# Optimization experiments

Measured on AMD Instinct MI355X. Metric: run time of the kernel, lower is better.

Reference implementation:

```python
import jax, jax.numpy as jnp
import numpy as np

N_HEAD = 16


def setup_inputs() -> dict:
    key = jax.random.key(0)
    k1, k2, k3 = jax.random.split(key, 3)
    B, T, C = 2, 2048, 1024
    x = jax.random.normal(k1, (B, T, C), dtype=jnp.float32)
    attention_mask = jnp.zeros((B, 1, 1, T), dtype=jnp.float32)
    W_attn = jax.random.normal(k2, (C, 3 * C), dtype=jnp.float32) * 0.02
    b_attn = jnp.zeros((3 * C,), dtype=jnp.float32)
    W_proj = jax.random.normal(k3, (C, C), dtype=jnp.float32) * 0.02
    b_proj = jnp.zeros((C,), dtype=jnp.float32)
    return {"x": x, "attention_mask": attention_mask, "W_attn": W_attn,
            "b_attn": b_attn, "W_proj": W_proj, "b_proj": b_proj}


def reference(x, attention_mask, W_attn, b_attn, W_proj, b_proj):
    B, T, C = x.shape
    H = N_HEAD
    d = C // H
    qkv = x @ W_attn + b_attn                      # [B, T, 3C]
    q, k, v = jnp.split(qkv, 3, axis=-1)
    q = q.reshape(B, T, H, d).transpose(0, 2, 1, 3)  # [B, H, T, d]
    k = k.reshape(B, T, H, d).transpose(0, 2, 1, 3)
    v = v.reshape(B, T, H, d).transpose(0, 2, 1, 3)
    att = jnp.einsum('bhtd,bhsd->bhts', q, k) * (1.0 / np.sqrt(d))
    causal = jnp.tril(jnp.ones((T, T), dtype=bool))
    att = jnp.where(causal[None, None], att, jnp.float32(-10000.0))
    att = att + attention_mask                     # additive broadcast mask
    att = jax.nn.softmax(att, axis=-1)             # dropout p=0.0 -> identity
    y = jnp.einsum('bhts,bhsd->bhtd', att, v)      # [B, H, T, d]
    y = y.transpose(0, 2, 1, 3).reshape(B, T, C)
    return y @ W_proj + b_proj
```

## Files before the change

### kernel.cpp

```cpp
#include <hip/hip_runtime.h>
#include <hip/hip_bf16.h>
#include <stdint.h>

#define BATCH 2
#define TT 2048
#define CC 1024
#define NH 16
#define HD 64

typedef __attribute__((ext_vector_type(8))) short short8;
typedef __attribute__((ext_vector_type(4))) short sh4;
typedef __attribute__((ext_vector_type(4))) float f32x4;
typedef __attribute__((ext_vector_type(2))) unsigned uint2v;

#define MFMA16 __builtin_amdgcn_mfma_f32_16x16x32_bf16
#define LOG2E 1.4426950408889634f

#if defined(__has_builtin)
#if __has_builtin(__builtin_amdgcn_exp2f)
#define EXP2(x) __builtin_amdgcn_exp2f(x)
#else
#define EXP2(x) __expf((x) * 0.6931471805599453f)
#endif
#else
#define EXP2(x) __expf((x) * 0.6931471805599453f)
#endif

__device__ __forceinline__ short f2bf(float f) {
  union { float f; unsigned u; } x;
  x.f = f;
  unsigned r = x.u + 0x7FFFu + ((x.u >> 16) & 1u);
  return (short)(r >> 16);
}

__device__ __forceinline__ void transpose_cast_tile(
    const float* __restrict__ W, short* __restrict__ Wt, int K, int N,
    int n0, int k0, int tid) {
  __shared__ __align__(16) float Ls[64][68];
  {
    const int r = tid >> 4, c4 = (tid & 15) * 4;
#pragma unroll
    for (int p = 0; p < 4; ++p) {
      const float4 v = *reinterpret_cast<const float4*>(
          &W[(size_t)(k0 + r + p * 16) * N + n0 + c4]);
      *reinterpret_cast<float4*>(&Ls[r + p * 16][c4]) = v;
    }
  }
  __syncthreads();
  {
    const int n = tid >> 2;
    const int kk0 = (tid & 3) * 16;
#pragma unroll
    for (int half = 0; half < 2; ++half) {
      short8 o;
#pragma unroll
      for (int t = 0; t < 8; ++t) o[t] = f2bf(Ls[kk0 + half * 8 + t][n]);
      *reinterpret_cast<short8*>(&Wt[(size_t)(n0 + n) * K + k0 + kk0 + half * 8]) = o;
    }
  }
}

__global__ __launch_bounds__(256) void prep_fused(
    const float* __restrict__ x, short* __restrict__ xb,
    const float* __restrict__ W_attn, short* __restrict__ wat,
    const float* __restrict__ W_proj, short* __restrict__ wpt,
    const float* __restrict__ mask, short* __restrict__ cb16,
    float* __restrict__ cf32) {
  const int blk = blockIdx.x;
  const int tid = threadIdx.x;
  if (blk < 2048) {
    const int i = (blk * 256 + tid) * 8;
    const float4 a = *reinterpret_cast<const float4*>(&x[i]);
    const float4 b = *reinterpret_cast<const float4*>(&x[i + 4]);
    short8 o;
    o[0] = f2bf(a.x); o[1] = f2bf(a.y); o[2] = f2bf(a.z); o[3] = f2bf(a.w);
    o[4] = f2bf(b.x); o[5] = f2bf(b.y); o[6] = f2bf(b.z); o[7] = f2bf(b.w);
    *reinterpret_cast<short8*>(&xb[i]) = o;
  } else if (blk < 2816) {
    const int b2 = blk - 2048;
    transpose_cast_tile(W_attn, wat, CC, 3 * CC, (b2 % 48) * 64,
                        (b2 / 48) * 64, tid);
  } else if (blk < 3072) {
    const int b3 = blk - 2816;
    transpose_cast_tile(W_proj, wpt, CC, CC, (b3 % 16) * 64, (b3 / 16) * 64,
                        tid);
  } else {
    const int b = blk - 3072;
    const int s = tid * 8;
    float c[8];
#pragma unroll
    for (int t = 0; t < 8; ++t) c[t] = __expf(mask[b * TT + s + t]);
    short8 o;
#pragma unroll
    for (int t = 0; t < 8; ++t) o[t] = f2bf(c[t]);
    *reinterpret_cast<short8*>(&cb16[b * TT + s]) = o;
#pragma unroll
    for (int t = 0; t < 8; ++t) cf32[b * TT + s + t] = c[t];
  }
}

template <bool OUT_BF16>
__device__ __forceinline__ void gemm_bt_body(
    const short* __restrict__ A, const short* __restrict__ Bt,
    const float* __restrict__ bias, void* __restrict__ C,
    short* __restrict__ vT, const float* __restrict__ cV, int M, int N, int K,
    int QS) {
  __shared__ __align__(16) short SM[24576];
  short* As = SM;
  short* Bs = SM + 8192;
  const int tid = threadIdx.x;
  const int w = tid >> 6, lane = tid & 63;
  const int quad = lane >> 4, l15 = lane & 15;
  const int m0 = blockIdx.y * 64, n0 = blockIdx.x * 128;

  f32x4 acc[4][2] = {};
  const int row16 = lane >> 2;
  const int c4 = (lane & 3) * 8;

  const int rbaseA = __builtin_amdgcn_readfirstlane(w * 16);
  const int rbaseB0 = __builtin_amdgcn_readfirstlane(w * 2 * 16);
  const int rbaseB1 = __builtin_amdgcn_readfirstlane((w * 2 + 1) * 16);

#define STAGE_TILE(buf, k0)                                                    \
  {                                                                            \
    _Pragma("unroll") for (int kh = 0; kh < 2; ++kh) {                         \
      const short* ga =                                                        \
          &A[(size_t)(m0 + rbaseA + row16) * K + (k0) + kh * 32 + c4];         \
      __builtin_amdgcn_global_load_lds(                                        \
          (const __attribute__((address_space(1))) void*)ga,                   \
          (__attribute__((address_space(3))) void*)                            \
              &As[(buf)*4096 + kh * 2048 + rbaseA * 32],                       \
          16, 0, 0);                                                           \
      const short* gb0 =                                                       \
          &Bt[(size_t)(n0 + rbaseB0 + row16) * K + (k0) + kh * 32 + c4];       \
      __builtin_amdgcn_global_load_lds(                                        \
          (const __attribute__((address_space(1))) void*)gb0,                  \
          (__attribute__((address_space(3))) void*)                            \
              &Bs[(buf)*8192 + kh * 4096 + rbaseB0 * 32],                      \
          16, 0, 0);                                                           \
      const short* gb1 =                                                       \
          &Bt[(size_t)(n0 + rbaseB1 + row16) * K + (k0) + kh * 32 + c4];       \
      __builtin_amdgcn_global_load_lds(                                        \
          (const __attribute__((address_space(1))) void*)gb1,                  \
          (__attribute__((address_space(3))) void*)                            \
              &Bs[(buf)*8192 + kh * 4096 + rbaseB1 * 32],                      \
          16, 0, 0);                                                           \
    }                                                                          \
  }

  STAGE_TILE(0, 0)
  __syncthreads();

  int cur = 0;
  for (int k0 = 0; k0 < K; k0 += 64) {
    if (k0 + 64 < K) STAGE_TILE(cur ^ 1, k0 + 64)

    short8 af[2][4], bfr[2][2];
#pragma unroll
    for (int kh = 0; kh < 2; ++kh) {
#pragma unroll
      for (int i = 0; i < 4; ++i)
        af[kh][i] = *reinterpret_cast<const short8*>(
            &As[cur * 4096 + kh * 2048 + (i * 16 + l15) * 32 + quad * 8]);
#pragma unroll
      for (int j = 0; j < 2; ++j)
        bfr[kh][j] = *reinterpret_cast<const short8*>(
            &Bs[cur * 8192 + kh * 4096 + (w * 32 + j * 16 + l15) * 32 +
                quad * 8]);
    }
#pragma unroll
    for (int kh = 0; kh < 2; ++kh)
#pragma unroll
      for (int i = 0; i < 4; ++i)
#pragma unroll
        for (int j = 0; j < 2; ++j)
          acc[i][j] = MFMA16(af[kh][i], bfr[kh][j], acc[i][j], 0, 0, 0);

    __syncthreads();
    cur ^= 1;
  }
#undef STAGE_TILE

  if (OUT_BF16 && vT != nullptr && n0 >= 2 * CC) {
    const int n0v = n0 - 2 * CC;
    const int b = m0 >> 11;
    const int s_batch = m0 & (TT - 1);
    short* Ls = SM;
#pragma unroll
    for (int i = 0; i < 4; ++i) {
      const int sl = i * 16 + quad * 4;
      const float4 cv = *reinterpret_cast<const float4*>(&cV[m0 + sl]);
      const float cvr[4] = {cv.x, cv.y, cv.z, cv.w};
#pragma unroll
      for (int j = 0; j < 2; ++j) {
        const int dl = w * 32 + j * 16 + l15;
        const float bb = bias[n0 + dl];
        sh4 pw;
#pragma unroll
        for (int r = 0; r < 4; ++r)
          pw[r] = f2bf((acc[i][j][r] + bb) * cvr[r]);
        *reinterpret_cast<sh4*>(&Ls[dl * 88 + sl]) = pw;
      }
    }
    __syncthreads();
    {
      const int row = tid >> 1, seg = tid & 1;
      const int bh = b * 16 + (n0v >> 6) + (row >> 6);
      const int d = row & 63;
      const short8* src = reinterpret_cast<const short8*>(&Ls[row * 88 + seg * 32]);
      short8* dst = reinterpret_cast<short8*>(
          &vT[((size_t)(bh * HD + d)) * TT + s_batch + seg * 32]);
#pragma unroll
      for (int t = 0; t < 4; ++t) dst[t] = src[t];
    }
    return;
  }

#pragma unroll
  for (int i = 0; i < 4; ++i) {
#pragma unroll
    for (int r = 0; r < 4; ++r) {
      const int row = m0 + i * 16 + quad * 4 + r;
#pragma unroll
      for (int j = 0; j < 2; ++j) {
        const int col = n0 + w * 32 + j * 16 + l15;
        float v = acc[i][j][r] + bias[col];
        if (col < QS) v *= 0.18033688011112042f;
        if (OUT_BF16)
          ((short*)C)[(size_t)row * N + col] = f2bf(v);
        else
          ((float*)C)[(size_t)row * N + col] = v;
      }
    }
  }
}

__global__ __launch_bounds__(256) void gemm_qkv(
    const short* __restrict__ A, const short* __restrict__ Bt,
    const float* __restrict__ bias, void* __restrict__ C,
    short* __restrict__ vT, const float* __restrict__ cV, int M, int N, int K,
    int QS) {
  gemm_bt_body<true>(A, Bt, bias, C, vT, cV, M, N, K, QS);
}

__global__ __launch_bounds__(256) void gemm_proj(
    const short* __restrict__ A, const short* __restrict__ Bt,
    const float* __restrict__ bias, void* __restrict__ C, int M, int N,
    int K) {
  gemm_bt_body<false>(A, Bt, bias, C, nullptr, nullptr, M, N, K, 0);
}

#define PST 72
__global__ __launch_bounds__(256) void attn_mfma10(
    const short* __restrict__ qkv, const short* __restrict__ vT,
    const short* __restrict__ cb16, short* __restrict__ y) {
  __shared__ __align__(16) short Ks[2][64 * PST];
  __shared__ __align__(16) short Vs[2][64 * PST];
  __shared__ __align__(16) short Ps[64 * PST];
  __shared__ __align__(16) short Cs[2][64];
  const int tid = threadIdx.x;
  const int w = tid >> 6, lane = tid & 63;
  const int quad = lane >> 4, l15 = lane & 15;
  const int bh = blockIdx.x, b = bh >> 4, h = bh & 15;
  const int px = blockIdx.y;
  const int qh = 31 - px;
  const int nth = qh + 1;
  const int ntot = nth + px + 1;
  const int RS = 3 * CC;

  int qt = qh;
  int qrow0 = qt * 64 + w * 16;

  short8 qf0, qf1;
  {
    const size_t qrow = (size_t)(b * TT + qrow0 + l15) * RS + h * HD + quad * 8;
    qf0 = *reinterpret_cast<const short8*>(&qkv[qrow]);
    qf1 = *reinterpret_cast<const short8*>(&qkv[qrow + 32]);
  }

  f32x4 l_acc = {};
  f32x4 o_acc[4] = {};

  const int sr = tid >> 3, sc = (tid & 7) * 8;
  const short* kbase = qkv + (size_t)(b * TT + sr) * RS + CC + h * HD + sc;
  const short* vbase = vT + (size_t)(bh * HD + sr) * TT + sc;
  const short* cbase = cb16 + b * TT;
  short* psrow = &Ps[(w * 16 + l15) * PST];
  const int kfo0 = quad * 8, kfo1 = 32 + quad * 8;

  short8 kpre0 = *reinterpret_cast<const short8*>(kbase);
  short8 kpre1 = *reinterpret_cast<const short8*>(kbase + (size_t)32 * RS);
  short8 vpre0 = *reinterpret_cast<const short8*>(vbase);
  short8 vpre1 = *reinterpret_cast<const short8*>(vbase + 32 * TT);
  short8 cpre = {};
  if (tid < 8) cpre = *reinterpret_cast<const short8*>(&cbase[tid * 8]);

  for (int it = 0; it < ntot; ++it) {
    const int kt = (it < nth) ? it : it - nth;
    const int s0 = kt * 64;

    if (it == nth) {
#pragma unroll
      for (int r = 0; r < 4; ++r) {
        const float inv = 1.0f / l_acc[r];
        const size_t row = (size_t)(b * TT + qrow0 + quad * 4 + r);
#pragma unroll
        for (int t = 0; t < 4; ++t)
          y[row * CC + h * HD + t * 16 + l15] = f2bf(o_acc[t][r] * inv);
      }
      qt = px;
      qrow0 = qt * 64 + w * 16;
      const size_t qrow = (size_t)(b * TT + qrow0 + l15) * RS + h * HD + quad * 8;
      qf0 = *reinterpret_cast<const short8*>(&qkv[qrow]);
      qf1 = *reinterpret_cast<const short8*>(&qkv[qrow + 32]);
      l_acc = f32x4{0.f, 0.f, 0.f, 0.f};
#pragma unroll
      for (int t = 0; t < 4; ++t) o_acc[t] = f32x4{0.f, 0.f, 0.f, 0.f};
    }

    const int cur = it & 1;
    *reinterpret_cast<short8*>(&Ks[cur][sr * PST + sc]) = kpre0;
    *reinterpret_cast<short8*>(&Ks[cur][(sr + 32) * PST + sc]) = kpre1;
    *reinterpret_cast<short8*>(&Vs[cur][sr * PST + sc]) = vpre0;
    *reinterpret_cast<short8*>(&Vs[cur][(sr + 32) * PST + sc]) = vpre1;
    if (tid < 8) *reinterpret_cast<short8*>(&Cs[cur][tid * 8]) = cpre;
    __syncthreads();

    if (it + 1 < ntot) {
      const int ktn = (it + 1 == nth) ? 0 : kt + 1;
      const short* kp = kbase + (size_t)ktn * 64 * RS;
      const short* vp = vbase + ktn * 64;
      kpre0 = *reinterpret_cast<const short8*>(kp);
      kpre1 = *reinterpret_cast<const short8*>(kp + (size_t)32 * RS);
      vpre0 = *reinterpret_cast<const short8*>(vp);
      vpre1 = *reinterpret_cast<const short8*>(vp + 32 * TT);
      if (tid < 8)
        cpre = *reinterpret_cast<const short8*>(&cbase[ktn * 64 + tid * 8]);
    }

    f32x4 sa[4] = {};
#pragma unroll
    for (int j = 0; j < 4; ++j) {
      const short8 kf0 = *reinterpret_cast<const short8*>(
          &Ks[cur][(j * 16 + l15) * PST + kfo0]);
      const short8 kf1 = *reinterpret_cast<const short8*>(
          &Ks[cur][(j * 16 + l15) * PST + kfo1]);
      sa[j] = MFMA16(kf0, qf0, sa[j], 0, 0, 0);
      sa[j] = MFMA16(kf1, qf1, sa[j], 0, 0, 0);
    }

    const bool boundary = (kt == qt);
    const int qg = qrow0 + l15;
#pragma unroll
    for (int j = 0; j < 4; ++j) {
      float pv[4];
#pragma unroll
      for (int r = 0; r < 4; ++r) {
        float v = sa[j][r];
        if (boundary) {
          const int sg = s0 + j * 16 + quad * 4 + r;
          if (sg > qg) v = -10000.0f;
        }
        pv[r] = EXP2(v);
      }
      union { __hip_bfloat162 h2[2]; uint2v u; } pk;
      pk.h2[0] = __float22bfloat162_rn(make_float2(pv[0], pv[1]));
      pk.h2[1] = __float22bfloat162_rn(make_float2(pv[2], pv[3]));
      *reinterpret_cast<uint2v*>(&psrow[j * 16 + quad * 4]) = pk.u;
    }

    const short8 pf0 = *reinterpret_cast<const short8*>(&psrow[kfo0]);
    const short8 pf1 = *reinterpret_cast<const short8*>(&psrow[kfo1]);
    const short8 cf0 = *reinterpret_cast<const short8*>(&Cs[cur][kfo0]);
    const short8 cf1 = *reinterpret_cast<const short8*>(&Cs[cur][kfo1]);
    l_acc = MFMA16(pf0, cf0, l_acc, 0, 0, 0);
    l_acc = MFMA16(pf1, cf1, l_acc, 0, 0, 0);
#pragma unroll
    for (int t = 0; t < 4; ++t) {
      const short8 vf0 = *reinterpret_cast<const short8*>(
          &Vs[cur][(t * 16 + l15) * PST + kfo0]);
      const short8 vf1 = *reinterpret_cast<const short8*>(
          &Vs[cur][(t * 16 + l15) * PST + kfo1]);
      o_acc[t] = MFMA16(pf0, vf0, o_acc[t], 0, 0, 0);
      o_acc[t] = MFMA16(pf1, vf1, o_acc[t], 0, 0, 0);
    }
  }

#pragma unroll
  for (int r = 0; r < 4; ++r) {
    const float inv = 1.0f / l_acc[r];
    const size_t row = (size_t)(b * TT + qrow0 + quad * 4 + r);
#pragma unroll
    for (int t = 0; t < 4; ++t)
      y[row * CC + h * HD + t * 16 + l15] = f2bf(o_acc[t][r] * inv);
  }
}

extern "C" void kernel_launch(void* const* d_in, const int* in_sizes, int n_in,
                              void* d_out, int out_size, void* d_ws,
                              size_t ws_size, hipStream_t stream) {
  const float* x = (const float*)d_in[0];
  const float* attn_mask = (const float*)d_in[1];
  const float* W_attn = (const float*)d_in[2];
  const float* b_attn = (const float*)d_in[3];
  const float* W_proj = (const float*)d_in[4];
  const float* b_proj = (const float*)d_in[5];
  float* out = (float*)d_out;

  const int M = BATCH * TT;

  short* xb = (short*)d_ws;
  short* wat = xb + (size_t)M * CC;
  short* wpt = wat + (size_t)(3 * CC) * CC;
  short* qkvb = wpt + (size_t)CC * CC;
  short* yb = qkvb + (size_t)M * 3 * CC;
  short* vTb = yb + (size_t)M * CC;
  short* cb16 = vTb + (size_t)BATCH * NH * HD * TT;
  float* cf32 = (float*)(cb16 + (size_t)BATCH * TT);

  prep_fused<<<3074, 256, 0, stream>>>(x, xb, W_attn, wat, W_proj, wpt,
                                       attn_mask, cb16, cf32);

  gemm_qkv<<<dim3((3 * CC) / 128, M / 64), 256, 0, stream>>>(
      xb, wat, b_attn, qkvb, vTb, cf32, M, 3 * CC, CC, CC);

  attn_mfma10<<<dim3(BATCH * NH, 16), 256, 0, stream>>>(
      qkvb, vTb, cb16, yb);

  gemm_proj<<<dim3(CC / 128, M / 64), 256, 0, stream>>>(
      yb, wpt, b_proj, out, M, CC, CC);
}
```

Measured before the change: 181.7 us.

## Software-pipeline attention: defer PV matmul one iteration behind QK and softmax

```diff
diff --git a/kernel.cpp b/kernel.cpp
--- a/kernel.cpp
+++ b/kernel.cpp
@@ -251,13 +251,13 @@
 }
 
 #define PST 72
-__global__ __launch_bounds__(256) void attn_mfma10(
+__global__ __launch_bounds__(256) void attn_mfma11(
     const short* __restrict__ qkv, const short* __restrict__ vT,
     const short* __restrict__ cb16, short* __restrict__ y) {
   __shared__ __align__(16) short Ks[2][64 * PST];
-  __shared__ __align__(16) short Vs[2][64 * PST];
-  __shared__ __align__(16) short Ps[64 * PST];
-  __shared__ __align__(16) short Cs[2][64];
+  __shared__ __align__(16) short Vs[3][64 * PST];
+  __shared__ __align__(16) short Ps[2][64 * PST];
+  __shared__ __align__(16) short Cs[3][64];
   const int tid = threadIdx.x;
   const int w = tid >> 6, lane = tid & 63;
   const int quad = lane >> 4, l15 = lane & 15;
@@ -285,8 +285,27 @@
   const short* kbase = qkv + (size_t)(b * TT + sr) * RS + CC + h * HD + sc;
   const short* vbase = vT + (size_t)(bh * HD + sr) * TT + sc;
   const short* cbase = cb16 + b * TT;
-  short* psrow = &Ps[(w * 16 + l15) * PST];
+  const int psoff = (w * 16 + l15) * PST;
   const int kfo0 = quad * 8, kfo1 = 32 + quad * 8;
+
+  auto pv_step = [&](int p2, int p3) {
+    const short* ppr = &Ps[p2][psoff];
+    const short8 pf0 = *reinterpret_cast<const short8*>(&ppr[kfo0]);
+    const short8 pf1 = *reinterpret_cast<const short8*>(&ppr[kfo1]);
+    const short8 cf0 = *reinterpret_cast<const short8*>(&Cs[p3][kfo0]);
+    const short8 cf1 = *reinterpret_cast<const short8*>(&Cs[p3][kfo1]);
+    l_acc = MFMA16(pf0, cf0, l_acc, 0, 0, 0);
+    l_acc = MFMA16(pf1, cf1, l_acc, 0, 0, 0);
+#pragma unroll
+    for (int t = 0; t < 4; ++t) {
+      const short8 vf0 = *reinterpret_cast<const short8*>(
+          &Vs[p3][(t * 16 + l15) * PST + kfo0]);
+      const short8 vf1 = *reinterpret_cast<const short8*>(
+          &Vs[p3][(t * 16 + l15) * PST + kfo1]);
+      o_acc[t] = MFMA16(pf0, vf0, o_acc[t], 0, 0, 0);
+      o_acc[t] = MFMA16(pf1, vf1, o_acc[t], 0, 0, 0);
+    }
+  };
 
   short8 kpre0 = *reinterpret_cast<const short8*>(kbase);
   short8 kpre1 = *reinterpret_cast<const short8*>(kbase + (size_t)32 * RS);
@@ -298,8 +317,17 @@
   for (int it = 0; it < ntot; ++it) {
     const int kt = (it < nth) ? it : it - nth;
     const int s0 = kt * 64;
+    const int cur2 = it & 1, cur3 = it % 3;
+    const int prv2 = cur2 ^ 1, prv3 = (it + 2) % 3;
+
+    *reinterpret_cast<short8*>(&Ks[cur2][sr * PST + sc]) = kpre0;
+    *reinterpret_cast<short8*>(&Ks[cur2][(sr + 32) * PST + sc]) = kpre1;
+    *reinterpret_cast<short8*>(&Vs[cur3][sr * PST + sc]) = vpre0;
+    *reinterpret_cast<short8*>(&Vs[cur3][(sr + 32) * PST + sc]) = vpre1;
+    if (tid < 8) *reinterpret_cast<short8*>(&Cs[cur3][tid * 8]) = cpre;
 
     if (it == nth) {
+      pv_step(prv2, prv3);
 #pragma unroll
       for (int r = 0; r < 4; ++r) {
         const float inv = 1.0f / l_acc[r];
@@ -317,13 +345,6 @@
 #pragma unroll
       for (int t = 0; t < 4; ++t) o_acc[t] = f32x4{0.f, 0.f, 0.f, 0.f};
     }
-
-    const int cur = it & 1;
-    *reinterpret_cast<short8*>(&Ks[cur][sr * PST + sc]) = kpre0;
-    *reinterpret_cast<short8*>(&Ks[cur][(sr + 32) * PST + sc]) = kpre1;
-    *reinterpret_cast<short8*>(&Vs[cur][sr * PST + sc]) = vpre0;
-    *reinterpret_cast<short8*>(&Vs[cur][(sr + 32) * PST + sc]) = vpre1;
-    if (tid < 8) *reinterpret_cast<short8*>(&Cs[cur][tid * 8]) = cpre;
     __syncthreads();
 
     if (it + 1 < ntot) {
@@ -342,15 +363,18 @@
 #pragma unroll
     for (int j = 0; j < 4; ++j) {
       const short8 kf0 = *reinterpret_cast<const short8*>(
-          &Ks[cur][(j * 16 + l15) * PST + kfo0]);
+          &Ks[cur2][(j * 16 + l15) * PST + kfo0]);
       const short8 kf1 = *reinterpret_cast<const short8*>(
-          &Ks[cur][(j * 16 + l15) * PST + kfo1]);
+          &Ks[cur2][(j * 16 + l15) * PST + kfo1]);
       sa[j] = MFMA16(kf0, qf0, sa[j], 0, 0, 0);
       sa[j] = MFMA16(kf1, qf1, sa[j], 0, 0, 0);
     }
 
+    if (it != nth && it > 0) pv_step(prv2, prv3);
+
     const bool boundary = (kt == qt);
     const int qg = qrow0 + l15;
+    short* psc = &Ps[cur2][psoff];
 #pragma unroll
     for (int j = 0; j < 4; ++j) {
       float pv[4];
@@ -366,26 +390,11 @@
       union { __hip_bfloat162 h2[2]; uint2v u; } pk;
       pk.h2[0] = __float22bfloat162_rn(make_float2(pv[0], pv[1]));
       pk.h2[1] = __float22bfloat162_rn(make_float2(pv[2], pv[3]));
-      *reinterpret_cast<uint2v*>(&psrow[j * 16 + quad * 4]) = pk.u;
-    }
-
-    const short8 pf0 = *reinterpret_cast<const short8*>(&psrow[kfo0]);
-    const short8 pf1 = *reinterpret_cast<const short8*>(&psrow[kfo1]);
-    const short8 cf0 = *reinterpret_cast<const short8*>(&Cs[cur][kfo0]);
-    const short8 cf1 = *reinterpret_cast<const short8*>(&Cs[cur][kfo1]);
-    l_acc = MFMA16(pf0, cf0, l_acc, 0, 0, 0);
-    l_acc = MFMA16(pf1, cf1, l_acc, 0, 0, 0);
-#pragma unroll
-    for (int t = 0; t < 4; ++t) {
-      const short8 vf0 = *reinterpret_cast<const short8*>(
-          &Vs[cur][(t * 16 + l15) * PST + kfo0]);
-      const short8 vf1 = *reinterpret_cast<const short8*>(
-          &Vs[cur][(t * 16 + l15) * PST + kfo1]);
-      o_acc[t] = MFMA16(pf0, vf0, o_acc[t], 0, 0, 0);
-      o_acc[t] = MFMA16(pf1, vf1, o_acc[t], 0, 0, 0);
-    }
-  }
-
+      *reinterpret_cast<uint2v*>(&psc[j * 16 + quad * 4]) = pk.u;
+    }
+  }
+
+  pv_step((ntot - 1) & 1, (ntot - 1) % 3);
 #pragma unroll
   for (int r = 0; r < 4; ++r) {
     const float inv = 1.0f / l_acc[r];
@@ -424,7 +433,7 @@
   gemm_qkv<<<dim3((3 * CC) / 128, M / 64), 256, 0, stream>>>(
       xb, wat, b_attn, qkvb, vTb, cf32, M, 3 * CC, CC, CC);
 
-  attn_mfma10<<<dim3(BATCH * NH, 16), 256, 0, stream>>>(
+  attn_mfma11<<<dim3(BATCH * NH, 16), 256, 0, stream>>>(
       qkvb, vTb, cb16, yb);
 
   gemm_proj<<<dim3(CC / 128, M / 64), 256, 0, stream>>>(
```

Measured after the change: 184.4 us. Within noise of the previous version (+1.5%).

## Load K/V fragments directly from global into registers, drop LDS staging

Applied to the files above, without the earlier changes.

```diff
diff --git a/kernel.cpp b/kernel.cpp
--- a/kernel.cpp
+++ b/kernel.cpp
@@ -251,13 +251,10 @@
 }
 
 #define PST 72
-__global__ __launch_bounds__(256) void attn_mfma10(
+__global__ __launch_bounds__(256) void attn_mfma12(
     const short* __restrict__ qkv, const short* __restrict__ vT,
     const short* __restrict__ cb16, short* __restrict__ y) {
-  __shared__ __align__(16) short Ks[2][64 * PST];
-  __shared__ __align__(16) short Vs[2][64 * PST];
   __shared__ __align__(16) short Ps[64 * PST];
-  __shared__ __align__(16) short Cs[2][64];
   const int tid = threadIdx.x;
   const int w = tid >> 6, lane = tid & 63;
   const int quad = lane >> 4, l15 = lane & 15;
@@ -281,19 +278,19 @@
   f32x4 l_acc = {};
   f32x4 o_acc[4] = {};
 
-  const int sr = tid >> 3, sc = (tid & 7) * 8;
-  const short* kbase = qkv + (size_t)(b * TT + sr) * RS + CC + h * HD + sc;
-  const short* vbase = vT + (size_t)(bh * HD + sr) * TT + sc;
-  const short* cbase = cb16 + b * TT;
+  const short* kgb = qkv + (size_t)b * TT * RS + CC + h * HD + quad * 8;
+  const short* vgb = vT + (size_t)bh * HD * TT + quad * 8;
+  const short* cgb = cb16 + b * TT + quad * 8;
   short* psrow = &Ps[(w * 16 + l15) * PST];
   const int kfo0 = quad * 8, kfo1 = 32 + quad * 8;
 
-  short8 kpre0 = *reinterpret_cast<const short8*>(kbase);
-  short8 kpre1 = *reinterpret_cast<const short8*>(kbase + (size_t)32 * RS);
-  short8 vpre0 = *reinterpret_cast<const short8*>(vbase);
-  short8 vpre1 = *reinterpret_cast<const short8*>(vbase + 32 * TT);
-  short8 cpre = {};
-  if (tid < 8) cpre = *reinterpret_cast<const short8*>(&cbase[tid * 8]);
+  short8 kf[4][2];
+#pragma unroll
+  for (int j = 0; j < 4; ++j) {
+    const short* kp = kgb + (size_t)(j * 16 + l15) * RS;
+    kf[j][0] = *reinterpret_cast<const short8*>(kp);
+    kf[j][1] = *reinterpret_cast<const short8*>(kp + 32);
+  }
 
   for (int it = 0; it < ntot; ++it) {
     const int kt = (it < nth) ? it : it - nth;
@@ -318,35 +315,31 @@
       for (int t = 0; t < 4; ++t) o_acc[t] = f32x4{0.f, 0.f, 0.f, 0.f};
     }
 
-    const int cur = it & 1;
-    *reinterpret_cast<short8*>(&Ks[cur][sr * PST + sc]) = kpre0;
-    *reinterpret_cast<short8*>(&Ks[cur][(sr + 32) * PST + sc]) = kpre1;
-    *reinterpret_cast<short8*>(&Vs[cur][sr * PST + sc]) = vpre0;
-    *reinterpret_cast<short8*>(&Vs[cur][(sr + 32) * PST + sc]) = vpre1;
-    if (tid < 8) *reinterpret_cast<short8*>(&Cs[cur][tid * 8]) = cpre;
-    __syncthreads();
+    short8 vf[4][2];
+#pragma unroll
+    for (int t = 0; t < 4; ++t) {
+      const short* vp = vgb + (size_t)(t * 16 + l15) * TT + s0;
+      vf[t][0] = *reinterpret_cast<const short8*>(vp);
+      vf[t][1] = *reinterpret_cast<const short8*>(vp + 32);
+    }
+    const short8 cf0 = *reinterpret_cast<const short8*>(cgb + s0);
+    const short8 cf1 = *reinterpret_cast<const short8*>(cgb + s0 + 32);
+
+    f32x4 sa[4] = {};
+#pragma unroll
+    for (int j = 0; j < 4; ++j) {
+      sa[j] = MFMA16(kf[j][0], qf0, sa[j], 0, 0, 0);
+      sa[j] = MFMA16(kf[j][1], qf1, sa[j], 0, 0, 0);
+    }
 
     if (it + 1 < ntot) {
       const int ktn = (it + 1 == nth) ? 0 : kt + 1;
-      const short* kp = kbase + (size_t)ktn * 64 * RS;
-      const short* vp = vbase + ktn * 64;
-      kpre0 = *reinterpret_cast<const short8*>(kp);
-      kpre1 = *reinterpret_cast<const short8*>(kp + (size_t)32 * RS);
-      vpre0 = *reinterpret_cast<const short8*>(vp);
-      vpre1 = *reinterpret_cast<const short8*>(vp + 32 * TT);
-      if (tid < 8)
-        cpre = *reinterpret_cast<const short8*>(&cbase[ktn * 64 + tid * 8]);
-    }
-
-    f32x4 sa[4] = {};
-#pragma unroll
-    for (int j = 0; j < 4; ++j) {
-      const short8 kf0 = *reinterpret_cast<const short8*>(
-          &Ks[cur][(j * 16 + l15) * PST + kfo0]);
-      const short8 kf1 = *reinterpret_cast<const short8*>(
-          &Ks[cur][(j * 16 + l15) * PST + kfo1]);
-      sa[j] = MFMA16(kf0, qf0, sa[j], 0, 0, 0);
-      sa[j] = MFMA16(kf1, qf1, sa[j], 0, 0, 0);
+#pragma unroll
+      for (int j = 0; j < 4; ++j) {
+        const short* kp = kgb + (size_t)(ktn * 64 + j * 16 + l15) * RS;
+        kf[j][0] = *reinterpret_cast<const short8*>(kp);
+        kf[j][1] = *reinterpret_cast<const short8*>(kp + 32);
+      }
     }
 
     const bool boundary = (kt == qt);
@@ -371,18 +364,12 @@
 
     const short8 pf0 = *reinterpret_cast<const short8*>(&psrow[kfo0]);
     const short8 pf1 = *reinterpret_cast<const short8*>(&psrow[kfo1]);
-    const short8 cf0 = *reinterpret_cast<const short8*>(&Cs[cur][kfo0]);
-    const short8 cf1 = *reinterpret_cast<const short8*>(&Cs[cur][kfo1]);
     l_acc = MFMA16(pf0, cf0, l_acc, 0, 0, 0);
     l_acc = MFMA16(pf1, cf1, l_acc, 0, 0, 0);
 #pragma unroll
     for (int t = 0; t < 4; ++t) {
-      const short8 vf0 = *reinterpret_cast<const short8*>(
-          &Vs[cur][(t * 16 + l15) * PST + kfo0]);
-      const short8 vf1 = *reinterpret_cast<const short8*>(
-          &Vs[cur][(t * 16 + l15) * PST + kfo1]);
-      o_acc[t] = MFMA16(pf0, vf0, o_acc[t], 0, 0, 0);
-      o_acc[t] = MFMA16(pf1, vf1, o_acc[t], 0, 0, 0);
+      o_acc[t] = MFMA16(pf0, vf[t][0], o_acc[t], 0, 0, 0);
+      o_acc[t] = MFMA16(pf1, vf[t][1], o_acc[t], 0, 0, 0);
     }
   }
 
@@ -424,7 +411,7 @@
   gemm_qkv<<<dim3((3 * CC) / 128, M / 64), 256, 0, stream>>>(
       xb, wat, b_attn, qkvb, vTb, cf32, M, 3 * CC, CC, CC);
 
-  attn_mfma10<<<dim3(BATCH * NH, 16), 256, 0, stream>>>(
+  attn_mfma12<<<dim3(BATCH * NH, 16), 256, 0, stream>>>(
       qkvb, vTb, cb16, yb);
 
   gemm_proj<<<dim3(CC / 128, M / 64), 256, 0, stream>>>(
```

New measurement: 262.2 us. 44.3% more time.

## Split attention waves into 2x2 query/key grid with shared-memory partial combine

Applied to the files above, without the earlier changes.

```diff
diff --git a/kernel.cpp b/kernel.cpp
--- a/kernel.cpp
+++ b/kernel.cpp
@@ -251,15 +251,17 @@
 }
 
 #define PST 72
-__global__ __launch_bounds__(256) void attn_mfma10(
+__global__ __launch_bounds__(256) void attn_mfma13(
     const short* __restrict__ qkv, const short* __restrict__ vT,
     const short* __restrict__ cb16, short* __restrict__ y) {
   __shared__ __align__(16) short Ks[2][64 * PST];
   __shared__ __align__(16) short Vs[2][64 * PST];
   __shared__ __align__(16) short Ps[64 * PST];
   __shared__ __align__(16) short Cs[2][64];
+  __shared__ float Lsc[64];
   const int tid = threadIdx.x;
   const int w = tid >> 6, lane = tid & 63;
+  const int qb = w >> 1, kb = w & 1;
   const int quad = lane >> 4, l15 = lane & 15;
   const int bh = blockIdx.x, b = bh >> 4, h = bh & 15;
   const int px = blockIdx.y;
@@ -269,24 +271,64 @@
   const int RS = 3 * CC;
 
   int qt = qh;
-  int qrow0 = qt * 64 + w * 16;
-
-  short8 qf0, qf1;
-  {
-    const size_t qrow = (size_t)(b * TT + qrow0 + l15) * RS + h * HD + quad * 8;
-    qf0 = *reinterpret_cast<const short8*>(&qkv[qrow]);
-    qf1 = *reinterpret_cast<const short8*>(&qkv[qrow + 32]);
-  }
-
-  f32x4 l_acc = {};
-  f32x4 o_acc[4] = {};
+  int qrow0b = qt * 64 + qb * 32;
+
+  short8 qf[2][2];
+#pragma unroll
+  for (int j = 0; j < 2; ++j) {
+    const size_t qrow =
+        (size_t)(b * TT + qrow0b + j * 16 + l15) * RS + h * HD + quad * 8;
+    qf[j][0] = *reinterpret_cast<const short8*>(&qkv[qrow]);
+    qf[j][1] = *reinterpret_cast<const short8*>(&qkv[qrow + 32]);
+  }
+
+  f32x4 l_acc[2] = {};
+  f32x4 o_acc[2][4] = {};
 
   const int sr = tid >> 3, sc = (tid & 7) * 8;
   const short* kbase = qkv + (size_t)(b * TT + sr) * RS + CC + h * HD + sc;
   const short* vbase = vT + (size_t)(bh * HD + sr) * TT + sc;
   const short* cbase = cb16 + b * TT;
-  short* psrow = &Ps[(w * 16 + l15) * PST];
-  const int kfo0 = quad * 8, kfo1 = 32 + quad * 8;
+
+  auto flush_combine = [&]() {
+    __syncthreads();
+    float* oscr = reinterpret_cast<float*>(&Ks[0][0]) + qb * (32 * 68);
+    if (kb == 1) {
+#pragma unroll
+      for (int j = 0; j < 2; ++j)
+#pragma unroll
+        for (int t = 0; t < 4; ++t)
+#pragma unroll
+          for (int r = 0; r < 4; ++r)
+            oscr[(j * 16 + quad * 4 + r) * 68 + t * 16 + l15] = o_acc[j][t][r];
+      if (l15 == 0) {
+#pragma unroll
+        for (int j = 0; j < 2; ++j)
+#pragma unroll
+          for (int r = 0; r < 4; ++r)
+            Lsc[qb * 32 + j * 16 + quad * 4 + r] = l_acc[j][r];
+      }
+    }
+    __syncthreads();
+    if (kb == 0) {
+#pragma unroll
+      for (int j = 0; j < 2; ++j) {
+#pragma unroll
+        for (int r = 0; r < 4; ++r) {
+          const float lsum = l_acc[j][r] + Lsc[qb * 32 + j * 16 + quad * 4 + r];
+          const float inv = 1.0f / lsum;
+          const size_t row = (size_t)(b * TT + qrow0b + j * 16 + quad * 4 + r);
+#pragma unroll
+          for (int t = 0; t < 4; ++t) {
+            const float v =
+                o_acc[j][t][r] + oscr[(j * 16 + quad * 4 + r) * 68 + t * 16 + l15];
+            y[row * CC + h * HD + t * 16 + l15] = f2bf(v * inv);
+          }
+        }
+      }
+    }
+    __syncthreads();
+  };
 
   short8 kpre0 = *reinterpret_cast<const short8*>(kbase);
   short8 kpre1 = *reinterpret_cast<const short8*>(kbase + (size_t)32 * RS);
@@ -300,22 +342,21 @@
     const int s0 = kt * 64;
 
     if (it == nth) {
-#pragma unroll
-      for (int r = 0; r < 4; ++r) {
-        const float inv = 1.0f / l_acc[r];
-        const size_t row = (size_t)(b * TT + qrow0 + quad * 4 + r);
-#pragma unroll
-        for (int t = 0; t < 4; ++t)
-          y[row * CC + h * HD + t * 16 + l15] = f2bf(o_acc[t][r] * inv);
-      }
+      flush_combine();
       qt = px;
-      qrow0 = qt * 64 + w * 16;
-      const size_t qrow = (size_t)(b * TT + qrow0 + l15) * RS + h * HD + quad * 8;
-      qf0 = *reinterpret_cast<const short8*>(&qkv[qrow]);
-      qf1 = *reinterpret_cast<const short8*>(&qkv[qrow + 32]);
-      l_acc = f32x4{0.f, 0.f, 0.f, 0.f};
-#pragma unroll
-      for (int t = 0; t < 4; ++t) o_acc[t] = f32x4{0.f, 0.f, 0.f, 0.f};
+      qrow0b = qt * 64 + qb * 32;
+#pragma unroll
+      for (int j = 0; j < 2; ++j) {
+        const size_t qrow =
+            (size_t)(b * TT + qrow0b + j * 16 + l15) * RS + h * HD + quad * 8;
+        qf[j][0] = *reinterpret_cast<const short8*>(&qkv[qrow]);
+        qf[j][1] = *reinterpret_cast<const short8*>(&qkv[qrow + 32]);
+      }
+      l_acc[0] = l_acc[1] = f32x4{0.f, 0.f, 0.f, 0.f};
+#pragma unroll
+      for (int j = 0; j < 2; ++j)
+#pragma unroll
+        for (int t = 0; t < 4; ++t) o_acc[j][t] = f32x4{0.f, 0.f, 0.f, 0.f};
     }
 
     const int cur = it & 1;
@@ -338,62 +379,64 @@
         cpre = *reinterpret_cast<const short8*>(&cbase[ktn * 64 + tid * 8]);
     }
 
-    f32x4 sa[4] = {};
-#pragma unroll
-    for (int j = 0; j < 4; ++j) {
+    f32x4 sa[2][2] = {};
+#pragma unroll
+    for (int i = 0; i < 2; ++i) {
       const short8 kf0 = *reinterpret_cast<const short8*>(
-          &Ks[cur][(j * 16 + l15) * PST + kfo0]);
+          &Ks[cur][(kb * 32 + i * 16 + l15) * PST + quad * 8]);
       const short8 kf1 = *reinterpret_cast<const short8*>(
-          &Ks[cur][(j * 16 + l15) * PST + kfo1]);
-      sa[j] = MFMA16(kf0, qf0, sa[j], 0, 0, 0);
-      sa[j] = MFMA16(kf1, qf1, sa[j], 0, 0, 0);
+          &Ks[cur][(kb * 32 + i * 16 + l15) * PST + 32 + quad * 8]);
+#pragma unroll
+      for (int j = 0; j < 2; ++j) {
+        sa[i][j] = MFMA16(kf0, qf[j][0], sa[i][j], 0, 0, 0);
+        sa[i][j] = MFMA16(kf1, qf[j][1], sa[i][j], 0, 0, 0);
+      }
     }
 
     const bool boundary = (kt == qt);
-    const int qg = qrow0 + l15;
-#pragma unroll
-    for (int j = 0; j < 4; ++j) {
-      float pv[4];
-#pragma unroll
-      for (int r = 0; r < 4; ++r) {
-        float v = sa[j][r];
-        if (boundary) {
-          const int sg = s0 + j * 16 + quad * 4 + r;
-          if (sg > qg) v = -10000.0f;
+#pragma unroll
+    for (int j = 0; j < 2; ++j) {
+      const int qg = qrow0b + j * 16 + l15;
+      short* psrow = &Ps[(size_t)(qb * 32 + j * 16 + l15) * PST];
+#pragma unroll
+      for (int i = 0; i < 2; ++i) {
+        float pv[4];
+#pragma unroll
+        for (int r = 0; r < 4; ++r) {
+          float v = sa[i][j][r];
+          if (boundary) {
+            const int sg = s0 + kb * 32 + i * 16 + quad * 4 + r;
+            if (sg > qg) v = -10000.0f;
+          }
+          pv[r] = EXP2(v);
         }
-        pv[r] = EXP2(v);
-      }
-      union { __hip_bfloat162 h2[2]; uint2v u; } pk;
-      pk.h2[0] = __float22bfloat162_rn(make_float2(pv[0], pv[1]));
-      pk.h2[1] = __float22bfloat162_rn(make_float2(pv[2], pv[3]));
-      *reinterpret_cast<uint2v*>(&psrow[j * 16 + quad * 4]) = pk.u;
-    }
-
-    const short8 pf0 = *reinterpret_cast<const short8*>(&psrow[kfo0]);
-    const short8 pf1 = *reinterpret_cast<const short8*>(&psrow[kfo1]);
-    const short8 cf0 = *reinterpret_cast<const short8*>(&Cs[cur][kfo0]);
-    const short8 cf1 = *reinterpret_cast<const short8*>(&Cs[cur][kfo1]);
-    l_acc = MFMA16(pf0, cf0, l_acc, 0, 0, 0);
-    l_acc = MFMA16(pf1, cf1, l_acc, 0, 0, 0);
+        union { __hip_bfloat162 h2[2]; uint2v u; } pk;
+        pk.h2[0] = __float22bfloat162_rn(make_float2(pv[0], pv[1]));
+        pk.h2[1] = __float22bfloat162_rn(make_float2(pv[2], pv[3]));
+        *reinterpret_cast<uint2v*>(&psrow[kb * 32 + i * 16 + quad * 4]) = pk.u;
+      }
+    }
+
+    const short8 cfr = *reinterpret_cast<const short8*>(
+        &Cs[cur][kb * 32 + quad * 8]);
+    short8 pf[2];
+#pragma unroll
+    for (int j = 0; j < 2; ++j) {
+      pf[j] = *reinterpret_cast<const short8*>(
+          &Ps[(size_t)(qb * 32 + j * 16 + l15) * PST + kb * 32 + quad * 8]);
+      l_acc[j] = MFMA16(pf[j], cfr, l_acc[j], 0, 0, 0);
+    }
 #pragma unroll
     for (int t = 0; t < 4; ++t) {
-      const short8 vf0 = *reinterpret_cast<const short8*>(
-          &Vs[cur][(t * 16 + l15) * PST + kfo0]);
-      const short8 vf1 = *reinterpret_cast<const short8*>(
-          &Vs[cur][(t * 16 + l15) * PST + kfo1]);
-      o_acc[t] = MFMA16(pf0, vf0, o_acc[t], 0, 0, 0);
-      o_acc[t] = MFMA16(pf1, vf1, o_acc[t], 0, 0, 0);
-    }
-  }
-
-#pragma unroll
-  for (int r = 0; r < 4; ++r) {
-    const float inv = 1.0f / l_acc[r];
-    const size_t row = (size_t)(b * TT + qrow0 + quad * 4 + r);
-#pragma unroll
-    for (int t = 0; t < 4; ++t)
-      y[row * CC + h * HD + t * 16 + l15] = f2bf(o_acc[t][r] * inv);
-  }
+      const short8 vf = *reinterpret_cast<const short8*>(
+          &Vs[cur][(t * 16 + l15) * PST + kb * 32 + quad * 8]);
+#pragma unroll
+      for (int j = 0; j < 2; ++j)
+        o_acc[j][t] = MFMA16(pf[j], vf, o_acc[j][t], 0, 0, 0);
+    }
+  }
+
+  flush_combine();
 }
 
 extern "C" void kernel_launch(void* const* d_in, const int* in_sizes, int n_in,
@@ -424,7 +467,7 @@
   gemm_qkv<<<dim3((3 * CC) / 128, M / 64), 256, 0, stream>>>(
       xb, wat, b_attn, qkvb, vTb, cf32, M, 3 * CC, CC, CC);
 
-  attn_mfma10<<<dim3(BATCH * NH, 16), 256, 0, stream>>>(
+  attn_mfma13<<<dim3(BATCH * NH, 16), 256, 0, stream>>>(
       qkvb, vTb, cb16, yb);
 
   gemm_proj<<<dim3(CC / 128, M / 64), 256, 0, stream>>>(
```

Result: no change. 181.2 us (-0.3%).
